# Optimization experiments

Measured on AMD Instinct MI355X. Metric: run time of the kernel, lower is better.

## Reference

```python
import jax, jax.numpy as jnp
import numpy as np

NUM_HEADS = 16
CHUNK = 128  # module's chunk_size; softmax is computed PER key-chunk (not globally) as in the source


def setup_inputs() -> dict:
    key = jax.random.key(0)
    ks = jax.random.split(key, 6)
    B, N, C = 2, 2048, 1024
    s = 0.02
    return {
        "x": jax.random.normal(ks[0], (B, N, C), dtype=jnp.float32),
        "Wq": jax.random.normal(ks[1], (C, C), dtype=jnp.float32) * s,
        "Wk": jax.random.normal(ks[2], (C, C), dtype=jnp.float32) * s,
        "Wv": jax.random.normal(ks[3], (C, C), dtype=jnp.float32) * s,
        "Wp": jax.random.normal(ks[4], (C, C), dtype=jnp.float32) * s,
        "bp": jnp.zeros((C,), dtype=jnp.float32),
    }


def reference(x, Wq, Wk, Wv, Wp, bp):
    B, N, C = x.shape
    H = NUM_HEADS
    D = C // H
    scale = jnp.asarray(D, x.dtype) ** -0.5
    # projections (no qkv bias)
    q = (x @ Wq).reshape(B, N, H, D).transpose(0, 2, 1, 3)  # [B,H,N,D]
    k = (x @ Wk).reshape(B, N, H, D).transpose(0, 2, 1, 3)
    v = (x @ Wv).reshape(B, N, H, D).transpose(0, 2, 1, 3)
    # split keys/values into chunks of CHUNK along sequence
    nk = N // CHUNK
    kc = k.reshape(B, H, nk, CHUNK, D)
    vc = v.reshape(B, H, nk, CHUNK, D)
    # scores per key chunk: [B,H,N,nk,CHUNK]
    scores = jnp.einsum('bhnd,bhkcd->bhnkc', q, kc) * scale
    # NOTE: faithful to the source, softmax normalizes within EACH key chunk only
    attn = jax.nn.softmax(scores, axis=-1)
    # accumulate over all key chunks (the += in the torch loop)
    out = jnp.einsum('bhnkc,bhkcd->bhnd', attn, vc)  # [B,H,N,D]
    out = out.transpose(0, 2, 1, 3).reshape(B, N, C)
    return out @ Wp + bp
```

## Files before the change

kernel.cpp:

```cpp
#include <hip/hip_runtime.h>
#include <hip/hip_bf16.h>


typedef __attribute__((ext_vector_type(4))) float f32x4;
typedef __attribute__((ext_vector_type(8))) short short8;

union U4S8 { uint4 u; short8 s; };

static __device__ __forceinline__ unsigned short f2bfu(float f) {
    union { __hip_bfloat16 b; unsigned short u; } cv;
    cv.b = __float2bfloat16(f);
    return cv.u;
}
static __device__ __forceinline__ __hip_bfloat16 f2bf(float f) {
    return __float2bfloat16(f);
}
static __device__ __forceinline__ unsigned int packbf(float a, float b) {
    return (unsigned int)f2bfu(a) | ((unsigned int)f2bfu(b) << 16);
}


__global__ void conv_x_kernel(const float* __restrict__ x, __hip_bfloat16* __restrict__ xb) {
    int i = blockIdx.x * 256 + threadIdx.x;
    float4 v = ((const float4*)x)[i];
    ushort4 o;
    o.x = f2bfu(v.x); o.y = f2bfu(v.y); o.z = f2bfu(v.z); o.w = f2bfu(v.w);
    ((ushort4*)xb)[i] = o;
}

__global__ void conv_wt_kernel(const float* __restrict__ w0, const float* __restrict__ w1,
                               const float* __restrict__ w2, const float* __restrict__ w3,
                               __hip_bfloat16* __restrict__ wt) {
    __shared__ float tile[32][33];
    const float* W = (blockIdx.z == 0) ? w0 : (blockIdx.z == 1) ? w1 : (blockIdx.z == 2) ? w2 : w3;
    __hip_bfloat16* out = wt + (size_t)blockIdx.z * 1048576;
    const int tx = threadIdx.x, ty = threadIdx.y;
    const int r0 = blockIdx.y * 32, c0 = blockIdx.x * 32;
    for (int j = 0; j < 4; ++j)
        tile[ty + j * 8][tx] = W[(size_t)(r0 + ty + j * 8) * 1024 + c0 + tx];
    __syncthreads();
    for (int j = 0; j < 4; ++j)
        out[(size_t)(c0 + ty + j * 8) * 1024 + r0 + tx] = f2bf(tile[tx][ty + j * 8]);
}

template <int MODE>
__global__ __launch_bounds__(256) void gemm_kernel(
    const __hip_bfloat16* __restrict__ A, const __hip_bfloat16* __restrict__ WT,
    __hip_bfloat16* __restrict__ q_ws, __hip_bfloat16* __restrict__ k_ws,
    __hip_bfloat16* __restrict__ vT_ws, float* __restrict__ outF,
    const float* __restrict__ bias) {
    const int t = threadIdx.x;
    const int lane = t & 63, w = t >> 6;
    const int quad = lane >> 4, l16 = lane & 15;
    const int wm = w >> 1, wn = w & 1;
    const int n0 = blockIdx.x * 128, m0 = blockIdx.y * 128;
    const int z = blockIdx.z;
    const __hip_bfloat16* Bt = WT + (size_t)z * 1048576;

    __shared__ __hip_bfloat16 As[128 * 48];
    __shared__ __hip_bfloat16 Bs[128 * 48];

    f32x4 acc[4][4];
    const f32x4 z4 = {0.f, 0.f, 0.f, 0.f};
    for (int i = 0; i < 4; ++i)
        for (int j = 0; j < 4; ++j) acc[i][j] = z4;

    for (int kk = 0; kk < 32; ++kk) {
        const int k0 = kk * 32;
        __syncthreads();
        for (int it = 0; it < 2; ++it) {
            int idx = it * 256 + t;
            int r = idx >> 2, sg = idx & 3;
            uint4 av = *(const uint4*)(A + (size_t)(m0 + r) * 1024 + k0 + sg * 8);
            *(uint4*)(As + r * 48 + sg * 8) = av;
            uint4 bv = *(const uint4*)(Bt + (size_t)(n0 + r) * 1024 + k0 + sg * 8);
            *(uint4*)(Bs + r * 48 + sg * 8) = bv;
        }
        __syncthreads();
        short8 af[4], bf[4];
        for (int i = 0; i < 4; ++i)
            af[i] = *(const short8*)(As + (wm * 64 + i * 16 + l16) * 48 + quad * 8);
        for (int j = 0; j < 4; ++j)
            bf[j] = *(const short8*)(Bs + (wn * 64 + j * 16 + l16) * 48 + quad * 8);
        for (int i = 0; i < 4; ++i)
            for (int j = 0; j < 4; ++j)
                acc[i][j] = __builtin_amdgcn_mfma_f32_16x16x32_bf16(af[i], bf[j], acc[i][j], 0, 0, 0);
    }

    const int r0 = m0 + wm * 64, c0 = n0 + wn * 64;
    if (MODE == 0) {
        if (z < 2) {
            const float sc = (z == 0) ? 0.18033688f : 1.0f;
            __hip_bfloat16* dst = (z == 0) ? q_ws : k_ws;
            for (int i = 0; i < 4; ++i) {
                int rowb = r0 + i * 16 + quad * 4;
                for (int j = 0; j < 4; ++j) {
                    int col = c0 + j * 16 + l16;
                    for (int rg = 0; rg < 4; ++rg)
                        dst[(size_t)(rowb + rg) * 1024 + col] = f2bf(acc[i][j][rg] * sc);
                }
            }
        } else {
            int b = r0 >> 11;
            for (int i = 0; i < 4; ++i) {
                int n_ = (r0 + i * 16 + quad * 4) & 2047;
                for (int j = 0; j < 4; ++j) {
                    int col = c0 + j * 16 + l16;
                    int h = col >> 6, d = col & 63;
                    ushort4 o;
                    o.x = f2bfu(acc[i][j][0]); o.y = f2bfu(acc[i][j][1]);
                    o.z = f2bfu(acc[i][j][2]); o.w = f2bfu(acc[i][j][3]);
                    *(ushort4*)(vT_ws + (size_t)((b * 16 + h) * 64 + d) * 2048 + n_) = o;
                }
            }
        }
    } else {
        for (int i = 0; i < 4; ++i) {
            int rowb = r0 + i * 16 + quad * 4;
            for (int j = 0; j < 4; ++j) {
                int col = c0 + j * 16 + l16;
                float bv = bias[col];
                for (int rg = 0; rg < 4; ++rg)
                    outF[(size_t)(rowb + rg) * 1024 + col] = acc[i][j][rg] + bv;
            }
        }
    }
}

__global__ __launch_bounds__(256, 4) void attn_kernel(
    const __hip_bfloat16* __restrict__ q_ws, const __hip_bfloat16* __restrict__ k_ws,
    const __hip_bfloat16* __restrict__ vT_ws, __hip_bfloat16* __restrict__ attn_ws) {
    const int t = threadIdx.x, lane = t & 63, w = t >> 6;
    const int quad = lane >> 4, l16 = lane & 15;
    const int qt = blockIdx.x;
    const int bh = blockIdx.y;
    const int b = bh >> 4, h = bh & 15;
    const int q0 = qt * 64;

    __shared__ __align__(16) char smem[35840];
    __hip_bfloat16* Ks = (__hip_bfloat16*)smem;
    __hip_bfloat16* Vt = (__hip_bfloat16*)(smem + 18432);
    __hip_bfloat16* T  = (__hip_bfloat16*)smem;

    short8 qf[2];
#pragma unroll
    for (int kt = 0; kt < 2; ++kt)
        qf[kt] = *(const short8*)(q_ws + (size_t)(b * 2048 + q0 + w * 16 + l16) * 1024 + h * 64 + kt * 32 + quad * 8);

    const f32x4 z4 = {0.f, 0.f, 0.f, 0.f};
    f32x4 O[4];
#pragma unroll
    for (int dt = 0; dt < 4; ++dt) O[dt] = z4;

    const int loLane = ((quad & 1) * 2) * 16 + l16;
    const int hiLane = loLane + 16;
    const bool topTile = quad >= 2;

    for (int ck = 0; ck < 16; ++ck) {
        __syncthreads();
#pragma unroll
        for (int it = 0; it < 4; ++it) {
            int idx = it * 256 + t;
            int r = idx >> 3, sg = idx & 7;
            uint4 v = *(const uint4*)(k_ws + (size_t)(b * 2048 + ck * 128 + r) * 1024 + h * 64 + sg * 8);
            *(uint4*)(Ks + r * 72 + sg * 8) = v;
        }
#pragma unroll
        for (int it = 0; it < 4; ++it) {
            int idx = it * 256 + t;
            int d = idx >> 4, sg = idx & 15;
            uint4 v = *(const uint4*)(vT_ws + (size_t)(bh * 64 + d) * 2048 + ck * 128 + sg * 8);
            *(uint4*)(Vt + d * 136 + sg * 8) = v;
        }
        __syncthreads();

        f32x4 s[8];
#pragma unroll
        for (int i = 0; i < 8; ++i) s[i] = z4;
#pragma unroll
        for (int kt = 0; kt < 2; ++kt)
#pragma unroll
            for (int i = 0; i < 8; ++i) {
                short8 kf = *(const short8*)(Ks + (i * 16 + l16) * 72 + kt * 32 + quad * 8);
                s[i] = __builtin_amdgcn_mfma_f32_16x16x32_bf16(kf, qf[kt], s[i], 0, 0, 0);
            }

        float sum = 0.f;
#pragma unroll
        for (int i = 0; i < 8; ++i) {
            f32x4 p;
            p[0] = __builtin_amdgcn_exp2f(s[i][0]);
            p[1] = __builtin_amdgcn_exp2f(s[i][1]);
            p[2] = __builtin_amdgcn_exp2f(s[i][2]);
            p[3] = __builtin_amdgcn_exp2f(s[i][3]);
            s[i] = p;
            sum += (p[0] + p[1]) + (p[2] + p[3]);
        }
        sum += __shfl_xor(sum, 16, 64);
        sum += __shfl_xor(sum, 32, 64);
        const float inv = 1.0f / sum;

        unsigned int pk[8][2];
#pragma unroll
        for (int i = 0; i < 8; ++i) {
            pk[i][0] = packbf(s[i][0] * inv, s[i][1] * inv);
            pk[i][1] = packbf(s[i][2] * inv, s[i][3] * inv);
        }

#pragma unroll
        for (int kt = 0; kt < 4; ++kt) {
            int a0 = (int)pk[2 * kt][0], a1 = (int)pk[2 * kt][1];
            int b0 = (int)pk[2 * kt + 1][0], b1 = (int)pk[2 * kt + 1][1];
            int e0 = __shfl(a0, loLane, 64), o0 = __shfl(b0, loLane, 64);
            int e1 = __shfl(a1, loLane, 64), o1 = __shfl(b1, loLane, 64);
            int e2 = __shfl(a0, hiLane, 64), o2 = __shfl(b0, hiLane, 64);
            int e3 = __shfl(a1, hiLane, 64), o3 = __shfl(b1, hiLane, 64);
            U4S8 bfr;
            bfr.u.x = (unsigned)(topTile ? o0 : e0);
            bfr.u.y = (unsigned)(topTile ? o1 : e1);
            bfr.u.z = (unsigned)(topTile ? o2 : e2);
            bfr.u.w = (unsigned)(topTile ? o3 : e3);
#pragma unroll
            for (int dt = 0; dt < 4; ++dt) {
                short8 vf = *(const short8*)(Vt + (dt * 16 + l16) * 136 + kt * 32 + quad * 8);
                O[dt] = __builtin_amdgcn_mfma_f32_16x16x32_bf16(vf, bfr.s, O[dt], 0, 0, 0);
            }
        }
    }

    __syncthreads();
#pragma unroll
    for (int dt = 0; dt < 4; ++dt) {
        unsigned int w0 = packbf(O[dt][0], O[dt][1]);
        unsigned int w1 = packbf(O[dt][2], O[dt][3]);
        int drow = dt * 16 + quad * 4;
        *(unsigned int*)(T + (w * 16 + l16) * 72 + drow) = w0;
        *(unsigned int*)(T + (w * 16 + l16) * 72 + drow + 2) = w1;
    }
    __syncthreads();
#pragma unroll
    for (int it = 0; it < 2; ++it) {
        int idx = it * 256 + t;
        int q = idx >> 3, seg = idx & 7;
        uint4 vv = *(const uint4*)(T + q * 72 + seg * 8);
        *(uint4*)(attn_ws + (size_t)(b * 2048 + q0 + q) * 1024 + h * 64 + seg * 8) = vv;
    }
}

extern "C" void kernel_launch(void* const* d_in, const int* in_sizes, int n_in,
                              void* d_out, int out_size, void* d_ws, size_t ws_size,
                              hipStream_t stream) {
    const float* x  = (const float*)d_in[0];
    const float* Wq = (const float*)d_in[1];
    const float* Wk = (const float*)d_in[2];
    const float* Wv = (const float*)d_in[3];
    const float* Wp = (const float*)d_in[4];
    const float* bp = (const float*)d_in[5];
    float* out = (float*)d_out;

    char* ws = (char*)d_ws;
    __hip_bfloat16* xb    = (__hip_bfloat16*)(ws);
    __hip_bfloat16* wT    = (__hip_bfloat16*)(ws + 8388608);
    __hip_bfloat16* q_ws  = (__hip_bfloat16*)(ws + 16777216);
    __hip_bfloat16* k_ws  = (__hip_bfloat16*)(ws + 25165824);
    __hip_bfloat16* vT_ws = (__hip_bfloat16*)(ws + 33554432);
    __hip_bfloat16* at_ws = (__hip_bfloat16*)(ws + 41943040);

    conv_x_kernel<<<4096, 256, 0, stream>>>(x, xb);
    conv_wt_kernel<<<dim3(32, 32, 4), dim3(32, 8), 0, stream>>>(Wq, Wk, Wv, Wp, wT);
    gemm_kernel<0><<<dim3(8, 32, 3), 256, 0, stream>>>(xb, wT, q_ws, k_ws, vT_ws, nullptr, nullptr);
    attn_kernel<<<dim3(32, 32), 256, 0, stream>>>(q_ws, k_ws, vT_ws, at_ws);
    gemm_kernel<1><<<dim3(8, 32, 1), 256, 0, stream>>>(at_ws, wT + 3 * 1048576, nullptr, nullptr, nullptr, out, bp);
}
```

Baseline: 227.3 us.

## Double-buffer attention K/V tiles, widen query tile, permute V layout, retile output GEMM

The attention kernel now handles 128 queries per block, with two 16-row M tiles per wave, so each K/V fragment load is reused twice. K/V chunks are double-buffered in LDS, and the next chunk is loaded while the current one is computed. The V workspace is written in a permuted column order so that the softmax probabilities in registers can be packed straight into MFMA B operands, which removes the cross-lane shuffles. The output projection gets its own 64x128-tile kernel to launch twice as many blocks. In exchange, attention uses twice the LDS, allows only 2 blocks per CU, launches half as many blocks and needs more registers.

```diff
diff --git a/kernel.cpp b/kernel.cpp
--- a/kernel.cpp
+++ b/kernel.cpp
@@ -43,12 +43,10 @@
         out[(size_t)(c0 + ty + j * 8) * 1024 + r0 + tx] = f2bf(tile[tx][ty + j * 8]);
 }
 
-template <int MODE>
-__global__ __launch_bounds__(256) void gemm_kernel(
+__global__ __launch_bounds__(256) void gemm_qkv_kernel(
     const __hip_bfloat16* __restrict__ A, const __hip_bfloat16* __restrict__ WT,
     __hip_bfloat16* __restrict__ q_ws, __hip_bfloat16* __restrict__ k_ws,
-    __hip_bfloat16* __restrict__ vT_ws, float* __restrict__ outF,
-    const float* __restrict__ bias) {
+    __hip_bfloat16* __restrict__ vT_ws) {
     const int t = threadIdx.x;
     const int lane = t & 63, w = t >> 6;
     const int quad = lane >> 4, l16 = lane & 15;
@@ -88,46 +86,89 @@
     }
 
     const int r0 = m0 + wm * 64, c0 = n0 + wn * 64;
-    if (MODE == 0) {
-        if (z < 2) {
-            const float sc = (z == 0) ? 0.18033688f : 1.0f;
-            __hip_bfloat16* dst = (z == 0) ? q_ws : k_ws;
-            for (int i = 0; i < 4; ++i) {
-                int rowb = r0 + i * 16 + quad * 4;
-                for (int j = 0; j < 4; ++j) {
-                    int col = c0 + j * 16 + l16;
-                    for (int rg = 0; rg < 4; ++rg)
-                        dst[(size_t)(rowb + rg) * 1024 + col] = f2bf(acc[i][j][rg] * sc);
-                }
-            }
-        } else {
-            int b = r0 >> 11;
-            for (int i = 0; i < 4; ++i) {
-                int n_ = (r0 + i * 16 + quad * 4) & 2047;
-                for (int j = 0; j < 4; ++j) {
-                    int col = c0 + j * 16 + l16;
-                    int h = col >> 6, d = col & 63;
-                    ushort4 o;
-                    o.x = f2bfu(acc[i][j][0]); o.y = f2bfu(acc[i][j][1]);
-                    o.z = f2bfu(acc[i][j][2]); o.w = f2bfu(acc[i][j][3]);
-                    *(ushort4*)(vT_ws + (size_t)((b * 16 + h) * 64 + d) * 2048 + n_) = o;
-                }
-            }
-        }
-    } else {
+    if (z < 2) {
+        const float sc = (z == 0) ? 0.18033688f : 1.0f;
+        __hip_bfloat16* dst = (z == 0) ? q_ws : k_ws;
         for (int i = 0; i < 4; ++i) {
             int rowb = r0 + i * 16 + quad * 4;
             for (int j = 0; j < 4; ++j) {
                 int col = c0 + j * 16 + l16;
-                float bv = bias[col];
                 for (int rg = 0; rg < 4; ++rg)
-                    outF[(size_t)(rowb + rg) * 1024 + col] = acc[i][j][rg] + bv;
-            }
-        }
-    }
-}
-
-__global__ __launch_bounds__(256, 4) void attn_kernel(
+                    dst[(size_t)(rowb + rg) * 1024 + col] = f2bf(acc[i][j][rg] * sc);
+            }
+        }
+    } else {
+        int b = r0 >> 11;
+        for (int i = 0; i < 4; ++i) {
+            int n_ = (r0 + i * 16 + quad * 4) & 2047;
+            int nb = n_ & ~127;
+            int c = n_ & 127;
+            int vcol = (c & ~31) | (((c >> 2) & 3) << 3) | (((c >> 4) & 1) << 2);
+            for (int j = 0; j < 4; ++j) {
+                int col = c0 + j * 16 + l16;
+                int h = col >> 6, d = col & 63;
+                ushort4 o;
+                o.x = f2bfu(acc[i][j][0]); o.y = f2bfu(acc[i][j][1]);
+                o.z = f2bfu(acc[i][j][2]); o.w = f2bfu(acc[i][j][3]);
+                *(ushort4*)(vT_ws + (size_t)((b * 16 + h) * 64 + d) * 2048 + nb + vcol) = o;
+            }
+        }
+    }
+}
+
+__global__ __launch_bounds__(256) void gemm_final_kernel(
+    const __hip_bfloat16* __restrict__ A, const __hip_bfloat16* __restrict__ Bt,
+    float* __restrict__ outF, const float* __restrict__ bias) {
+    const int t = threadIdx.x;
+    const int lane = t & 63, w = t >> 6;
+    const int quad = lane >> 4, l16 = lane & 15;
+    const int n0 = blockIdx.x * 128, m0 = blockIdx.y * 64;
+
+    __shared__ __hip_bfloat16 As[64 * 48];
+    __shared__ __hip_bfloat16 Bs[128 * 48];
+
+    f32x4 acc[4][2];
+    const f32x4 z4 = {0.f, 0.f, 0.f, 0.f};
+    for (int i = 0; i < 4; ++i)
+        for (int j = 0; j < 2; ++j) acc[i][j] = z4;
+
+    for (int kk = 0; kk < 32; ++kk) {
+        const int k0 = kk * 32;
+        __syncthreads();
+        {
+            int r = t >> 2, sg = t & 3;
+            uint4 av = *(const uint4*)(A + (size_t)(m0 + r) * 1024 + k0 + sg * 8);
+            *(uint4*)(As + r * 48 + sg * 8) = av;
+        }
+        for (int it = 0; it < 2; ++it) {
+            int idx = it * 256 + t;
+            int r = idx >> 2, sg = idx & 3;
+            uint4 bv = *(const uint4*)(Bt + (size_t)(n0 + r) * 1024 + k0 + sg * 8);
+            *(uint4*)(Bs + r * 48 + sg * 8) = bv;
+        }
+        __syncthreads();
+        short8 af[4], bf[2];
+        for (int i = 0; i < 4; ++i)
+            af[i] = *(const short8*)(As + (i * 16 + l16) * 48 + quad * 8);
+        for (int j = 0; j < 2; ++j)
+            bf[j] = *(const short8*)(Bs + (w * 32 + j * 16 + l16) * 48 + quad * 8);
+        for (int i = 0; i < 4; ++i)
+            for (int j = 0; j < 2; ++j)
+                acc[i][j] = __builtin_amdgcn_mfma_f32_16x16x32_bf16(af[i], bf[j], acc[i][j], 0, 0, 0);
+    }
+
+    for (int i = 0; i < 4; ++i) {
+        int rowb = m0 + i * 16 + quad * 4;
+        for (int j = 0; j < 2; ++j) {
+            int col = n0 + w * 32 + j * 16 + l16;
+            float bv = bias[col];
+            for (int rg = 0; rg < 4; ++rg)
+                outF[(size_t)(rowb + rg) * 1024 + col] = acc[i][j][rg] + bv;
+        }
+    }
+}
+
+__global__ __launch_bounds__(256, 2) void attn_kernel(
     const __hip_bfloat16* __restrict__ q_ws, const __hip_bfloat16* __restrict__ k_ws,
     const __hip_bfloat16* __restrict__ vT_ws, __hip_bfloat16* __restrict__ attn_ws) {
     const int t = threadIdx.x, lane = t & 63, w = t >> 6;
@@ -135,111 +176,140 @@
     const int qt = blockIdx.x;
     const int bh = blockIdx.y;
     const int b = bh >> 4, h = bh & 15;
-    const int q0 = qt * 64;
-
-    __shared__ __align__(16) char smem[35840];
-    __hip_bfloat16* Ks = (__hip_bfloat16*)smem;
-    __hip_bfloat16* Vt = (__hip_bfloat16*)(smem + 18432);
-    __hip_bfloat16* T  = (__hip_bfloat16*)smem;
-
-    short8 qf[2];
-#pragma unroll
-    for (int kt = 0; kt < 2; ++kt)
-        qf[kt] = *(const short8*)(q_ws + (size_t)(b * 2048 + q0 + w * 16 + l16) * 1024 + h * 64 + kt * 32 + quad * 8);
+    const int q0 = qt * 128;
+
+    __shared__ __align__(16) char smem[71680];
+
+    short8 qf[2][2];
+#pragma unroll
+    for (int mt = 0; mt < 2; ++mt)
+#pragma unroll
+        for (int kt = 0; kt < 2; ++kt)
+            qf[mt][kt] = *(const short8*)(q_ws + (size_t)(b * 2048 + q0 + w * 32 + mt * 16 + l16) * 1024 + h * 64 + kt * 32 + quad * 8);
 
     const f32x4 z4 = {0.f, 0.f, 0.f, 0.f};
-    f32x4 O[4];
-#pragma unroll
-    for (int dt = 0; dt < 4; ++dt) O[dt] = z4;
-
-    const int loLane = ((quad & 1) * 2) * 16 + l16;
-    const int hiLane = loLane + 16;
-    const bool topTile = quad >= 2;
-
-    for (int ck = 0; ck < 16; ++ck) {
-        __syncthreads();
+    f32x4 O[2][4];
+#pragma unroll
+    for (int mt = 0; mt < 2; ++mt)
+#pragma unroll
+        for (int dt = 0; dt < 4; ++dt) O[mt][dt] = z4;
+
+    {
+        __hip_bfloat16* Ksb = (__hip_bfloat16*)(smem);
+        __hip_bfloat16* Vtb = (__hip_bfloat16*)(smem + 18432);
 #pragma unroll
         for (int it = 0; it < 4; ++it) {
             int idx = it * 256 + t;
             int r = idx >> 3, sg = idx & 7;
-            uint4 v = *(const uint4*)(k_ws + (size_t)(b * 2048 + ck * 128 + r) * 1024 + h * 64 + sg * 8);
-            *(uint4*)(Ks + r * 72 + sg * 8) = v;
+            uint4 v = *(const uint4*)(k_ws + (size_t)(b * 2048 + r) * 1024 + h * 64 + sg * 8);
+            *(uint4*)(Ksb + r * 72 + sg * 8) = v;
         }
 #pragma unroll
         for (int it = 0; it < 4; ++it) {
             int idx = it * 256 + t;
             int d = idx >> 4, sg = idx & 15;
-            uint4 v = *(const uint4*)(vT_ws + (size_t)(bh * 64 + d) * 2048 + ck * 128 + sg * 8);
-            *(uint4*)(Vt + d * 136 + sg * 8) = v;
-        }
-        __syncthreads();
-
-        f32x4 s[8];
-#pragma unroll
-        for (int i = 0; i < 8; ++i) s[i] = z4;
+            uint4 v = *(const uint4*)(vT_ws + (size_t)(bh * 64 + d) * 2048 + sg * 8);
+            *(uint4*)(Vtb + d * 136 + sg * 8) = v;
+        }
+    }
+    __syncthreads();
+
+    for (int ck = 0; ck < 16; ++ck) {
+        const int cur = ck & 1;
+        __hip_bfloat16* Ks = (__hip_bfloat16*)(smem + cur * 35840);
+        __hip_bfloat16* Vt = (__hip_bfloat16*)(smem + cur * 35840 + 18432);
+
+        if (ck + 1 < 16) {
+            __hip_bfloat16* Ksn = (__hip_bfloat16*)(smem + (cur ^ 1) * 35840);
+            __hip_bfloat16* Vtn = (__hip_bfloat16*)(smem + (cur ^ 1) * 35840 + 18432);
+            const int nk0 = (ck + 1) * 128;
+#pragma unroll
+            for (int it = 0; it < 4; ++it) {
+                int idx = it * 256 + t;
+                int r = idx >> 3, sg = idx & 7;
+                uint4 v = *(const uint4*)(k_ws + (size_t)(b * 2048 + nk0 + r) * 1024 + h * 64 + sg * 8);
+                *(uint4*)(Ksn + r * 72 + sg * 8) = v;
+            }
+#pragma unroll
+            for (int it = 0; it < 4; ++it) {
+                int idx = it * 256 + t;
+                int d = idx >> 4, sg = idx & 15;
+                uint4 v = *(const uint4*)(vT_ws + (size_t)(bh * 64 + d) * 2048 + nk0 + sg * 8);
+                *(uint4*)(Vtn + d * 136 + sg * 8) = v;
+            }
+        }
+
+        f32x4 s[2][8];
+#pragma unroll
+        for (int mt = 0; mt < 2; ++mt)
+#pragma unroll
+            for (int i = 0; i < 8; ++i) s[mt][i] = z4;
 #pragma unroll
         for (int kt = 0; kt < 2; ++kt)
 #pragma unroll
             for (int i = 0; i < 8; ++i) {
                 short8 kf = *(const short8*)(Ks + (i * 16 + l16) * 72 + kt * 32 + quad * 8);
-                s[i] = __builtin_amdgcn_mfma_f32_16x16x32_bf16(kf, qf[kt], s[i], 0, 0, 0);
-            }
-
-        float sum = 0.f;
-#pragma unroll
-        for (int i = 0; i < 8; ++i) {
-            f32x4 p;
-            p[0] = __builtin_amdgcn_exp2f(s[i][0]);
-            p[1] = __builtin_amdgcn_exp2f(s[i][1]);
-            p[2] = __builtin_amdgcn_exp2f(s[i][2]);
-            p[3] = __builtin_amdgcn_exp2f(s[i][3]);
-            s[i] = p;
-            sum += (p[0] + p[1]) + (p[2] + p[3]);
-        }
-        sum += __shfl_xor(sum, 16, 64);
-        sum += __shfl_xor(sum, 32, 64);
-        const float inv = 1.0f / sum;
-
-        unsigned int pk[8][2];
-#pragma unroll
-        for (int i = 0; i < 8; ++i) {
-            pk[i][0] = packbf(s[i][0] * inv, s[i][1] * inv);
-            pk[i][1] = packbf(s[i][2] * inv, s[i][3] * inv);
+                s[0][i] = __builtin_amdgcn_mfma_f32_16x16x32_bf16(kf, qf[0][kt], s[0][i], 0, 0, 0);
+                s[1][i] = __builtin_amdgcn_mfma_f32_16x16x32_bf16(kf, qf[1][kt], s[1][i], 0, 0, 0);
+            }
+
+#pragma unroll
+        for (int mt = 0; mt < 2; ++mt) {
+            float sum = 0.f;
+#pragma unroll
+            for (int i = 0; i < 8; ++i) {
+                f32x4 p;
+                p[0] = __builtin_amdgcn_exp2f(s[mt][i][0]);
+                p[1] = __builtin_amdgcn_exp2f(s[mt][i][1]);
+                p[2] = __builtin_amdgcn_exp2f(s[mt][i][2]);
+                p[3] = __builtin_amdgcn_exp2f(s[mt][i][3]);
+                s[mt][i] = p;
+                sum += (p[0] + p[1]) + (p[2] + p[3]);
+            }
+            sum += __shfl_xor(sum, 16, 64);
+            sum += __shfl_xor(sum, 32, 64);
+            const float inv = 1.0f / sum;
+#pragma unroll
+            for (int i = 0; i < 8; ++i) {
+                s[mt][i][0] *= inv; s[mt][i][1] *= inv;
+                s[mt][i][2] *= inv; s[mt][i][3] *= inv;
+            }
         }
 
 #pragma unroll
         for (int kt = 0; kt < 4; ++kt) {
-            int a0 = (int)pk[2 * kt][0], a1 = (int)pk[2 * kt][1];
-            int b0 = (int)pk[2 * kt + 1][0], b1 = (int)pk[2 * kt + 1][1];
-            int e0 = __shfl(a0, loLane, 64), o0 = __shfl(b0, loLane, 64);
-            int e1 = __shfl(a1, loLane, 64), o1 = __shfl(b1, loLane, 64);
-            int e2 = __shfl(a0, hiLane, 64), o2 = __shfl(b0, hiLane, 64);
-            int e3 = __shfl(a1, hiLane, 64), o3 = __shfl(b1, hiLane, 64);
-            U4S8 bfr;
-            bfr.u.x = (unsigned)(topTile ? o0 : e0);
-            bfr.u.y = (unsigned)(topTile ? o1 : e1);
-            bfr.u.z = (unsigned)(topTile ? o2 : e2);
-            bfr.u.w = (unsigned)(topTile ? o3 : e3);
+            U4S8 bfr[2];
+#pragma unroll
+            for (int mt = 0; mt < 2; ++mt) {
+                bfr[mt].u.x = packbf(s[mt][2 * kt][0], s[mt][2 * kt][1]);
+                bfr[mt].u.y = packbf(s[mt][2 * kt][2], s[mt][2 * kt][3]);
+                bfr[mt].u.z = packbf(s[mt][2 * kt + 1][0], s[mt][2 * kt + 1][1]);
+                bfr[mt].u.w = packbf(s[mt][2 * kt + 1][2], s[mt][2 * kt + 1][3]);
+            }
 #pragma unroll
             for (int dt = 0; dt < 4; ++dt) {
                 short8 vf = *(const short8*)(Vt + (dt * 16 + l16) * 136 + kt * 32 + quad * 8);
-                O[dt] = __builtin_amdgcn_mfma_f32_16x16x32_bf16(vf, bfr.s, O[dt], 0, 0, 0);
-            }
-        }
-    }
-
+                O[0][dt] = __builtin_amdgcn_mfma_f32_16x16x32_bf16(vf, bfr[0].s, O[0][dt], 0, 0, 0);
+                O[1][dt] = __builtin_amdgcn_mfma_f32_16x16x32_bf16(vf, bfr[1].s, O[1][dt], 0, 0, 0);
+            }
+        }
+        __syncthreads();
+    }
+
+    __hip_bfloat16* T = (__hip_bfloat16*)smem;
+#pragma unroll
+    for (int mt = 0; mt < 2; ++mt)
+#pragma unroll
+        for (int dt = 0; dt < 4; ++dt) {
+            unsigned int w0 = packbf(O[mt][dt][0], O[mt][dt][1]);
+            unsigned int w1 = packbf(O[mt][dt][2], O[mt][dt][3]);
+            int drow = dt * 16 + quad * 4;
+            *(unsigned int*)(T + (w * 32 + mt * 16 + l16) * 72 + drow) = w0;
+            *(unsigned int*)(T + (w * 32 + mt * 16 + l16) * 72 + drow + 2) = w1;
+        }
     __syncthreads();
 #pragma unroll
-    for (int dt = 0; dt < 4; ++dt) {
-        unsigned int w0 = packbf(O[dt][0], O[dt][1]);
-        unsigned int w1 = packbf(O[dt][2], O[dt][3]);
-        int drow = dt * 16 + quad * 4;
-        *(unsigned int*)(T + (w * 16 + l16) * 72 + drow) = w0;
-        *(unsigned int*)(T + (w * 16 + l16) * 72 + drow + 2) = w1;
-    }
-    __syncthreads();
-#pragma unroll
-    for (int it = 0; it < 2; ++it) {
+    for (int it = 0; it < 4; ++it) {
         int idx = it * 256 + t;
         int q = idx >> 3, seg = idx & 7;
         uint4 vv = *(const uint4*)(T + q * 72 + seg * 8);
@@ -268,7 +338,7 @@
 
     conv_x_kernel<<<4096, 256, 0, stream>>>(x, xb);
     conv_wt_kernel<<<dim3(32, 32, 4), dim3(32, 8), 0, stream>>>(Wq, Wk, Wv, Wp, wT);
-    gemm_kernel<0><<<dim3(8, 32, 3), 256, 0, stream>>>(xb, wT, q_ws, k_ws, vT_ws, nullptr, nullptr);
-    attn_kernel<<<dim3(32, 32), 256, 0, stream>>>(q_ws, k_ws, vT_ws, at_ws);
-    gemm_kernel<1><<<dim3(8, 32, 1), 256, 0, stream>>>(at_ws, wT + 3 * 1048576, nullptr, nullptr, nullptr, out, bp);
-}
+    gemm_qkv_kernel<<<dim3(8, 32, 3), 256, 0, stream>>>(xb, wT, q_ws, k_ws, vT_ws);
+    attn_kernel<<<dim3(16, 32), 256, 0, stream>>>(q_ws, k_ws, vT_ws, at_ws);
+    gemm_final_kernel<<<dim3(8, 64), 256, 0, stream>>>(at_ws, wT + 3 * 1048576, out, bp);
+}
```

Result: faster. 195.5 us (-14.0%).
